# Performance work log

Hardware: AMD Instinct MI355X
Metric: run time of the kernel (lower is better)

## Reference

```python
import jax, jax.numpy as jnp
import numpy as np

B, T, H = 16, 2048, 1024   # batch, time, hidden_dim
G, V, D = 2, 320, 128      # num_codebooks, codebook_size, codebook_dim
TAU = 1.0                  # gumbel-softmax temperature (forward default)
EPS = 1e-9


def setup_inputs() -> dict:
    key = jax.random.key(0)
    ks = jax.random.split(key, 6)
    return {
        "x": jax.random.normal(ks[0], (B, T, H), jnp.float32),
        "W_in": jax.random.normal(ks[1], (G * V, H), jnp.float32) / np.sqrt(H),
        "b_in": jnp.zeros((G * V,), jnp.float32),
        "codebook": jax.random.uniform(ks[2], (G, V, D), jnp.float32),
        "W_out": jax.random.normal(ks[3], (H, G * D), jnp.float32) / np.sqrt(G * D),
        "b_out": jnp.zeros((H,), jnp.float32),
        "gumbel_u": jax.random.uniform(ks[4], (B, T, G, V), jnp.float32,
                                       minval=1e-6, maxval=1.0 - 1e-6),
    }


def reference(x, W_in, b_in, codebook, W_out, b_out, gumbel_u):
    # input projection -> per-group logits [B,T,G,V]
    logits = (x @ W_in.T + b_in).reshape(B, T, G, V)
    # gumbel-softmax (soft, training path)
    gumbels = -jnp.log(-jnp.log(gumbel_u))
    probs = jax.nn.softmax((logits + gumbels) / TAU, axis=-1)
    # perplexity over average code usage
    avg_probs = probs.mean(axis=(0, 1))  # [G,V]
    perplexity = jnp.exp(-(avg_probs * jnp.log(avg_probs + EPS)).sum(-1)).mean()
    # quantize: soft mixture over codebook, concat groups, project out
    q = jnp.einsum('btgv,gvd->btgd', probs, codebook).reshape(B, T, G * D)
    q = q @ W_out.T + b_out  # [B,T,H]
    commit_loss = jnp.mean((x - jax.lax.stop_gradient(q)) ** 2)
    return (q, perplexity, commit_loss)
```

## Files before the change

kernel.cpp:

```cpp
#include <hip/hip_runtime.h>

typedef unsigned short ushort_t;
typedef unsigned int uint_t;
typedef __attribute__((ext_vector_type(4))) float f32x4;
typedef __attribute__((ext_vector_type(8))) short bf16x8;

#define B_   16
#define T_   2048
#define H_   1024
#define G_   2
#define V_   320
#define D_   128
#define NT   32768
#define GV   640
#define GD   256

#define LGKM0() asm volatile("s_waitcnt lgkmcnt(0)" ::: "memory")
#define BAR()   __builtin_amdgcn_s_barrier()
#define GLDS16(g, l) __builtin_amdgcn_global_load_lds( \
    (const __attribute__((address_space(1))) void*)(g), \
    (__attribute__((address_space(3))) void*)(l), 16, 0, 0)

__device__ __forceinline__ ushort_t cvt_bf16(float f) {
  uint_t u = __float_as_uint(f);
  uint_t r = (u + 0x7FFFu + ((u >> 16) & 1u)) >> 16;
  return (ushort_t)r;
}

__device__ __forceinline__ bf16x8 pack8(f32x4 a, f32x4 b) {
  union { uint_t u[4]; bf16x8 v; } r;
  asm("v_cvt_pk_bf16_f32 %0, %1, %2" : "=v"(r.u[0]) : "v"(a[0]), "v"(a[1]));
  asm("v_cvt_pk_bf16_f32 %0, %1, %2" : "=v"(r.u[1]) : "v"(a[2]), "v"(a[3]));
  asm("v_cvt_pk_bf16_f32 %0, %1, %2" : "=v"(r.u[2]) : "v"(b[0]), "v"(b[1]));
  asm("v_cvt_pk_bf16_f32 %0, %1, %2" : "=v"(r.u[3]) : "v"(b[2]), "v"(b[3]));
  return r.v;
}

__global__ void pq_prep(const float* __restrict__ W_in, const float* __restrict__ W_out,
                        const float* __restrict__ cb, ushort_t* __restrict__ winb,
                        ushort_t* __restrict__ woutb, ushort_t* __restrict__ cbp,
                        float* __restrict__ avg_g, float* __restrict__ closs,
                        uint_t* __restrict__ counter) {
  int idx = blockIdx.x * 256 + threadIdx.x;
  const int N1 = GV * H_;
  const int N2 = H_ * GD;
  const int N3 = 81920;
  if (idx < N1) { winb[idx] = cvt_bf16(W_in[idx]); return; }
  idx -= N1;
  if (idx < N2) { woutb[idx] = cvt_bf16(W_out[idx]); return; }
  idx -= N2;
  if (idx < N3) {
    int g = idx / 40960;
    int r = idx % 40960;
    int kk = r / 4096;
    int r2 = r % 4096;
    int n  = r2 >> 9;
    int ln = (r2 >> 3) & 63;
    int i  = r2 & 7;
    int v = kk * 32 + (ln >> 4) * 8 + i;
    int d = n * 16 + (ln & 15);
    cbp[idx] = cvt_bf16(cb[((size_t)g * V_ + v) * D_ + d]);
    return;
  }
  idx -= N3;
  if (idx < GV) { avg_g[idx] = 0.f; return; }
  idx -= GV;
  if (idx == 0) { *closs = 0.f; *counter = 0u; }
}

__global__ __launch_bounds__(512, 2) void pq_kA(
    const float* __restrict__ x, const float* __restrict__ b_in,
    const float* __restrict__ gum, const ushort_t* __restrict__ winb,
    const ushort_t* __restrict__ cbp, ushort_t* __restrict__ qmid,
    float* __restrict__ avg_g) {
  __shared__ char smem[117248];
  char* sAbuf = smem;
  char* sBbuf = smem + 32768;
  char* sP    = smem;
  float* sAvg = (float*)(smem + 114688);

  const int tid = threadIdx.x;
  const int lane = tid & 63;
  const int wid = tid >> 6;
  const int wm = wid >> 1;
  const int g  = wid & 1;
  const int lo = lane & 15;
  const int hi = lane >> 4;
  const int row0 = blockIdx.x * 128;

  for (int i = tid; i < GV; i += 512) sAvg[i] = 0.f;

  const int aR   = (wid << 4) + (lane >> 3);
  const int aCc  = (lane & 7) ^ (lane >> 3);
  const float* aSrc0 = x + (size_t)(row0 + aR) * H_ + aCc * 4;
  const int bV   = wid * 80 + (lane >> 2);
  const int bCc  = (lane & 3) ^ ((lane >> 3) & 3);
  const ushort_t* bSrc0 = winb + (size_t)bV * H_ + bCc * 8;

  f32x4 acc[2][20];
#pragma unroll
  for (int m = 0; m < 2; ++m)
#pragma unroll
    for (int n = 0; n < 20; ++n) acc[m][n] = (f32x4){0.f, 0.f, 0.f, 0.f};

  __syncthreads();

#define STAGE(buf, kb)                                                          \
  do {                                                                          \
    char* la = sAbuf + (buf) * 16384 + wid * 2048;                              \
    char* lb = sBbuf + (buf) * 40960 + wid * 5120;                              \
    const float* as = aSrc0 + (kb);                                             \
    GLDS16(as,            la);                                                  \
    GLDS16(as + 8 * H_,   la + 1024);                                           \
    const ushort_t* bs = bSrc0 + (kb);                                          \
    GLDS16(bs,             lb);                                                 \
    GLDS16(bs + 16 * H_,   lb + 1024);                                          \
    GLDS16(bs + 32 * H_,   lb + 2048);                                          \
    GLDS16(bs + 48 * H_,   lb + 3072);                                          \
    GLDS16(bs + 64 * H_,   lb + 4096);                                          \
  } while (0)

  STAGE(0, 0);

  const int swzA = lo & 7;
  const int swzB = (lo >> 1) & 3;

#pragma unroll 1
  for (int ks = 0; ks < 32; ++ks) {
    const int cur = ks & 1;
    if (ks < 31) {
      STAGE(cur ^ 1, (ks + 1) * 32);
      asm volatile("s_waitcnt vmcnt(7)" ::: "memory");
    } else {
      asm volatile("s_waitcnt vmcnt(0)" ::: "memory");
    }
    BAR();

    const char* cA = sAbuf + cur * 16384;
    const char* cB = sBbuf + cur * 40960;
    bf16x8 af[2];
#pragma unroll
    for (int m = 0; m < 2; ++m) {
      const int row = wm * 32 + m * 16 + lo;
      const int rb = row * 128;
      f32x4 a0 = *reinterpret_cast<const f32x4*>(cA + rb + (((hi * 2)     ^ swzA) * 16));
      f32x4 a1 = *reinterpret_cast<const f32x4*>(cA + rb + (((hi * 2 + 1) ^ swzA) * 16));
      af[m] = pack8(a0, a1);
    }
#pragma unroll
    for (int n = 0; n < 20; ++n) {
      const int v = g * 320 + n * 16 + lo;
      bf16x8 bf = *reinterpret_cast<const bf16x8*>(cB + v * 64 + ((hi ^ swzB) * 16));
      acc[0][n] = __builtin_amdgcn_mfma_f32_16x16x32_bf16(af[0], bf, acc[0][n], 0, 0, 0);
      acc[1][n] = __builtin_amdgcn_mfma_f32_16x16x32_bf16(af[1], bf, acc[1][n], 0, 0, 0);
    }
    LGKM0();
    BAR();
  }
#undef STAGE

  float bias[20];
#pragma unroll
  for (int n = 0; n < 20; ++n) bias[n] = b_in[g * 320 + n * 16 + lo];

#pragma unroll
  for (int mrep = 0; mrep < 2; ++mrep) {
#pragma unroll
    for (int j = 0; j < 4; ++j) {
      const int trow = row0 + wm * 32 + mrep * 16 + hi * 4 + j;
      const float* up = gum + ((size_t)trow * G_ + g) * V_;
      float zmax = -3.0e38f;
#pragma unroll
      for (int n = 0; n < 20; ++n) {
        float u = up[n * 16 + lo];
        float gv = -__logf(-__logf(u));
        float z = acc[mrep][n][j] + bias[n] + gv;
        acc[mrep][n][j] = z;
        zmax = fmaxf(zmax, z);
      }
#pragma unroll
      for (int mk = 1; mk <= 8; mk <<= 1) zmax = fmaxf(zmax, __shfl_xor(zmax, mk));
      float s = 0.f;
#pragma unroll
      for (int n = 0; n < 20; ++n) {
        float p = __expf(acc[mrep][n][j] - zmax);
        acc[mrep][n][j] = p;
        s += p;
      }
#pragma unroll
      for (int mk = 1; mk <= 8; mk <<= 1) s += __shfl_xor(s, mk);
      float inv = 1.f / s;
#pragma unroll
      for (int n = 0; n < 20; ++n) acc[mrep][n][j] *= inv;
    }
#pragma unroll
    for (int n = 0; n < 20; ++n) {
      float cs = acc[mrep][n][0] + acc[mrep][n][1] + acc[mrep][n][2] + acc[mrep][n][3];
      cs += __shfl_xor(cs, 16);
      cs += __shfl_xor(cs, 32);
      if (hi == 0) atomicAdd(&sAvg[g * 320 + n * 16 + lo], cs);
    }
#pragma unroll
    for (int n = 0; n < 20; ++n) {
#pragma unroll
      for (int j = 0; j < 4; ++j) {
        float v = acc[mrep][n][j];
        float pv = __shfl_xor(v, 1);
        if ((lane & 1) == 0) {
          uint_t w = (uint_t)cvt_bf16(v) | ((uint_t)cvt_bf16(pv) << 16);
          int prow = wm * 16 + hi * 4 + j;
          int byte = (prow * 1280 + (g * 320 + n * 16 + lo) * 2) ^ ((prow & 7) << 4);
          *reinterpret_cast<uint_t*>(sP + byte) = w;
        }
      }
    }
    LGKM0();
    f32x4 acc2[8];
#pragma unroll
    for (int n = 0; n < 8; ++n) acc2[n] = (f32x4){0.f, 0.f, 0.f, 0.f};
#pragma unroll
    for (int kk = 0; kk < 10; ++kk) {
      int prow = wm * 16 + lo;
      int byte = (prow * 1280 + g * 640 + kk * 64 + hi * 16) ^ ((prow & 7) << 4);
      bf16x8 ap = *reinterpret_cast<const bf16x8*>(sP + byte);
#pragma unroll
      for (int n = 0; n < 8; ++n) {
        bf16x8 bc = *reinterpret_cast<const bf16x8*>(cbp + ((size_t)((g * 10 + kk) * 8 + n) * 64 + lane) * 8);
        acc2[n] = __builtin_amdgcn_mfma_f32_16x16x32_bf16(ap, bc, acc2[n], 0, 0, 0);
      }
    }
#pragma unroll
    for (int n = 0; n < 8; ++n) {
#pragma unroll
      for (int j = 0; j < 4; ++j) {
        float v = acc2[n][j];
        float pv = __shfl_xor(v, 1);
        if ((lane & 1) == 0) {
          uint_t w = (uint_t)cvt_bf16(v) | ((uint_t)cvt_bf16(pv) << 16);
          int trow = row0 + wm * 32 + mrep * 16 + hi * 4 + j;
          *reinterpret_cast<uint_t*>(qmid + (size_t)trow * GD + g * 128 + n * 16 + lo) = w;
        }
      }
    }
  }
  __syncthreads();
  for (int i = tid; i < GV; i += 512) atomicAdd(&avg_g[i], sAvg[i]);
}

__global__ __launch_bounds__(512, 2) void pq_kB(
    const ushort_t* __restrict__ qmid, const ushort_t* __restrict__ woutb,
    const float* __restrict__ b_out, const float* __restrict__ x,
    float* __restrict__ out, float* __restrict__ closs,
    const float* __restrict__ avg_g, uint_t* __restrict__ counter) {
  __shared__ char smem[49152 + 64];
  __shared__ int sLast;
  char* sA = smem;
  char* sB = smem + 16384;
  float* sRed = (float*)(smem + 49152);

  const int tid = threadIdx.x;
  const int lane = tid & 63;
  const int wid = tid >> 6;
  const int wm = wid >> 2;
  const int wn = wid & 3;
  const int lo = lane & 15, hi = lane >> 4;
  const int tm = blockIdx.x >> 2;
  const int tn = blockIdx.x & 3;
  const int row0 = tm * 128;
  const int col0 = tn * 256;

  f32x4 acc[4][4];
#pragma unroll
  for (int mr = 0; mr < 4; ++mr)
#pragma unroll
    for (int nr = 0; nr < 4; ++nr) acc[mr][nr] = (f32x4){0.f, 0.f, 0.f, 0.f};

  for (int ks = 0; ks < 4; ++ks) {
    const int kb = ks * 64;
#pragma unroll
    for (int u = 0; u < 2; ++u) {
      int s = u * 512 + tid;
      int r = s >> 3, c = s & 7;
      uint4 wv = *reinterpret_cast<const uint4*>(qmid + (size_t)(row0 + r) * GD + kb + c * 8);
      int byte = (r * 128 + c * 16) ^ ((r & 7) << 4);
      *reinterpret_cast<uint4*>(sA + byte) = wv;
    }
#pragma unroll
    for (int u = 0; u < 4; ++u) {
      int s = u * 512 + tid;
      int r = s >> 3, c = s & 7;
      uint4 wv = *reinterpret_cast<const uint4*>(woutb + (size_t)(col0 + r) * GD + kb + c * 8);
      int byte = (r * 128 + c * 16) ^ ((r & 7) << 4);
      *reinterpret_cast<uint4*>(sB + byte) = wv;
    }
    __syncthreads();
#pragma unroll
    for (int kk = 0; kk < 2; ++kk) {
      bf16x8 af[4], bf[4];
#pragma unroll
      for (int mr = 0; mr < 4; ++mr) {
        int row = wm * 64 + mr * 16 + lo;
        int byte = (row * 128 + kk * 64 + hi * 16) ^ ((row & 7) << 4);
        af[mr] = *reinterpret_cast<const bf16x8*>(sA + byte);
      }
#pragma unroll
      for (int nr = 0; nr < 4; ++nr) {
        int col = wn * 64 + nr * 16 + lo;
        int byte = (col * 128 + kk * 64 + hi * 16) ^ ((col & 7) << 4);
        bf[nr] = *reinterpret_cast<const bf16x8*>(sB + byte);
      }
#pragma unroll
      for (int mr = 0; mr < 4; ++mr)
#pragma unroll
        for (int nr = 0; nr < 4; ++nr)
          acc[mr][nr] = __builtin_amdgcn_mfma_f32_16x16x32_bf16(af[mr], bf[nr], acc[mr][nr], 0, 0, 0);
    }
    __syncthreads();
  }
  float bias[4];
#pragma unroll
  for (int nr = 0; nr < 4; ++nr) bias[nr] = b_out[col0 + wn * 64 + nr * 16 + lo];
  float csum = 0.f;
#pragma unroll
  for (int mr = 0; mr < 4; ++mr)
#pragma unroll
    for (int nr = 0; nr < 4; ++nr)
#pragma unroll
      for (int j = 0; j < 4; ++j) {
        int row = row0 + wm * 64 + mr * 16 + hi * 4 + j;
        int col = col0 + wn * 64 + nr * 16 + lo;
        float q = acc[mr][nr][j] + bias[nr];
        out[(size_t)row * H_ + col] = q;
        float d = x[(size_t)row * H_ + col] - q;
        csum += d * d;
      }
#pragma unroll
  for (int mk = 1; mk <= 32; mk <<= 1) csum += __shfl_xor(csum, mk);
  if (lane == 0) sRed[wid] = csum;
  __syncthreads();
  if (tid == 0) {
    float t = 0.f;
    for (int w = 0; w < 8; ++w) t += sRed[w];
    atomicAdd(closs, t);
    __threadfence();
    uint_t c = atomicAdd(counter, 1u);
    sLast = (c == 1023u) ? 1 : 0;
  }
  __syncthreads();
  if (sLast && tid < 64) {
    float a0 = 0.f, a1 = 0.f;
    for (int v = tid; v < V_; v += 64) {
      float p0 = avg_g[v] * (1.f / (float)NT);
      a0 += p0 * __logf(p0 + 1e-9f);
      float p1 = avg_g[V_ + v] * (1.f / (float)NT);
      a1 += p1 * __logf(p1 + 1e-9f);
    }
#pragma unroll
    for (int mk = 1; mk <= 32; mk <<= 1) { a0 += __shfl_xor(a0, mk); a1 += __shfl_xor(a1, mk); }
    if (tid == 0) {
      float cl = atomicAdd(closs, 0.0f);
      out[(size_t)NT * H_]     = 0.5f * (__expf(-a0) + __expf(-a1));
      out[(size_t)NT * H_ + 1] = cl * (1.f / ((float)NT * (float)H_));
    }
  }
}

extern "C" void kernel_launch(void* const* d_in, const int* in_sizes, int n_in,
                              void* d_out, int out_size, void* d_ws, size_t ws_size,
                              hipStream_t stream) {
  const float* x     = (const float*)d_in[0];
  const float* W_in  = (const float*)d_in[1];
  const float* b_in  = (const float*)d_in[2];
  const float* cb    = (const float*)d_in[3];
  const float* W_out = (const float*)d_in[4];
  const float* b_out = (const float*)d_in[5];
  const float* gum   = (const float*)d_in[6];
  float* out = (float*)d_out;

  char* ws = (char*)d_ws;
  ushort_t* winb  = (ushort_t*)ws;
  ushort_t* woutb = (ushort_t*)(ws + 1310720);
  ushort_t* cbp   = (ushort_t*)(ws + 1835008);
  float*    avg_g = (float*)(ws + 1998848);
  float*    closs = (float*)(ws + 2001408);
  uint_t*   cnt   = (uint_t*)(ws + 2001472);
  ushort_t* qmid  = (ushort_t*)(ws + 2001920);

  pq_prep<<<3907, 256, 0, stream>>>(W_in, W_out, cb, winb, woutb, cbp, avg_g, closs, cnt);
  pq_kA<<<256, 512, 0, stream>>>(x, b_in, gum, winb, cbp, qmid, avg_g);
  pq_kB<<<1024, 512, 0, stream>>>(qmid, woutb, b_out, x, out, closs, avg_g, cnt);
}
```

Baseline: 235.5 us.

## Load x tiles directly into registers and triple-buffer the W_in LDS stages

The x operand of the input GEMM now goes from global memory straight into registers, one k-step ahead, instead of through a swizzled LDS staging buffer. The freed LDS space triple-buffers the bf16 W_in tiles, so B loads run two k-steps ahead under adjusted vmcnt waits. This is meant to cut LDS traffic and give the B operand more latency hiding. In exchange, each x prefetch must land within one iteration, the per-lane strided global reads may coalesce less well, and the larger LDS footprint may limit occupancy.

```diff
diff --git a/kernel.cpp b/kernel.cpp
--- a/kernel.cpp
+++ b/kernel.cpp
@@ -73,11 +73,10 @@
     const float* __restrict__ gum, const ushort_t* __restrict__ winb,
     const ushort_t* __restrict__ cbp, ushort_t* __restrict__ qmid,
     float* __restrict__ avg_g) {
-  __shared__ char smem[117248];
-  char* sAbuf = smem;
-  char* sBbuf = smem + 32768;
+  __shared__ char smem[125440];
+  char* sBbuf = smem;
   char* sP    = smem;
-  float* sAvg = (float*)(smem + 114688);
+  float* sAvg = (float*)(smem + 122880);
 
   const int tid = threadIdx.x;
   const int lane = tid & 63;
@@ -90,13 +89,13 @@
 
   for (int i = tid; i < GV; i += 512) sAvg[i] = 0.f;
 
-  const int aR   = (wid << 4) + (lane >> 3);
-  const int aCc  = (lane & 7) ^ (lane >> 3);
-  const float* aSrc0 = x + (size_t)(row0 + aR) * H_ + aCc * 4;
   const int bV   = wid * 80 + (lane >> 2);
   const int bCc  = (lane & 3) ^ ((lane >> 3) & 3);
   const ushort_t* bSrc0 = winb + (size_t)bV * H_ + bCc * 8;
 
+  const float* xr0 = x + (size_t)(row0 + wm * 32 + lo) * H_ + hi * 8;
+  const float* xr1 = xr0 + (size_t)16 * H_;
+
   f32x4 acc[2][20];
 #pragma unroll
   for (int m = 0; m < 2; ++m)
@@ -105,13 +104,9 @@
 
   __syncthreads();
 
-#define STAGE(buf, kb)                                                          \
+#define STAGEB(buf, kb)                                                         \
   do {                                                                          \
-    char* la = sAbuf + (buf) * 16384 + wid * 2048;                              \
     char* lb = sBbuf + (buf) * 40960 + wid * 5120;                              \
-    const float* as = aSrc0 + (kb);                                             \
-    GLDS16(as,            la);                                                  \
-    GLDS16(as + 8 * H_,   la + 1024);                                           \
     const ushort_t* bs = bSrc0 + (kb);                                          \
     GLDS16(bs,             lb);                                                 \
     GLDS16(bs + 16 * H_,   lb + 1024);                                          \
@@ -120,44 +115,45 @@
     GLDS16(bs + 64 * H_,   lb + 4096);                                          \
   } while (0)
 
-  STAGE(0, 0);
-
-  const int swzA = lo & 7;
+  STAGEB(0, 0);
+  f32x4 xa0 = *reinterpret_cast<const f32x4*>(xr0);
+  f32x4 xa1 = *reinterpret_cast<const f32x4*>(xr0 + 4);
+  f32x4 xb0 = *reinterpret_cast<const f32x4*>(xr1);
+  f32x4 xb1 = *reinterpret_cast<const f32x4*>(xr1 + 4);
+  STAGEB(1, 32);
+
   const int swzB = (lo >> 1) & 3;
 
 #pragma unroll 1
   for (int ks = 0; ks < 32; ++ks) {
-    const int cur = ks & 1;
+    if (ks < 31) asm volatile("s_waitcnt vmcnt(5)" ::: "memory");
+    else         asm volatile("s_waitcnt vmcnt(0)" ::: "memory");
+    BAR();
+
+    bf16x8 af0 = pack8(xa0, xa1);
+    bf16x8 af1 = pack8(xb0, xb1);
+
     if (ks < 31) {
-      STAGE(cur ^ 1, (ks + 1) * 32);
-      asm volatile("s_waitcnt vmcnt(7)" ::: "memory");
-    } else {
-      asm volatile("s_waitcnt vmcnt(0)" ::: "memory");
-    }
-    BAR();
-
-    const char* cA = sAbuf + cur * 16384;
-    const char* cB = sBbuf + cur * 40960;
-    bf16x8 af[2];
-#pragma unroll
-    for (int m = 0; m < 2; ++m) {
-      const int row = wm * 32 + m * 16 + lo;
-      const int rb = row * 128;
-      f32x4 a0 = *reinterpret_cast<const f32x4*>(cA + rb + (((hi * 2)     ^ swzA) * 16));
-      f32x4 a1 = *reinterpret_cast<const f32x4*>(cA + rb + (((hi * 2 + 1) ^ swzA) * 16));
-      af[m] = pack8(a0, a1);
-    }
+      const int ko = (ks + 1) * 32;
+      xa0 = *reinterpret_cast<const f32x4*>(xr0 + ko);
+      xa1 = *reinterpret_cast<const f32x4*>(xr0 + ko + 4);
+      xb0 = *reinterpret_cast<const f32x4*>(xr1 + ko);
+      xb1 = *reinterpret_cast<const f32x4*>(xr1 + ko + 4);
+      if (ks < 30) STAGEB((ks + 2) % 3, (ks + 2) * 32);
+    }
+
+    const char* cB = sBbuf + (ks % 3) * 40960;
 #pragma unroll
     for (int n = 0; n < 20; ++n) {
       const int v = g * 320 + n * 16 + lo;
       bf16x8 bf = *reinterpret_cast<const bf16x8*>(cB + v * 64 + ((hi ^ swzB) * 16));
-      acc[0][n] = __builtin_amdgcn_mfma_f32_16x16x32_bf16(af[0], bf, acc[0][n], 0, 0, 0);
-      acc[1][n] = __builtin_amdgcn_mfma_f32_16x16x32_bf16(af[1], bf, acc[1][n], 0, 0, 0);
+      acc[0][n] = __builtin_amdgcn_mfma_f32_16x16x32_bf16(af0, bf, acc[0][n], 0, 0, 0);
+      acc[1][n] = __builtin_amdgcn_mfma_f32_16x16x32_bf16(af1, bf, acc[1][n], 0, 0, 0);
     }
     LGKM0();
     BAR();
   }
-#undef STAGE
+#undef STAGEB
 
   float bias[20];
 #pragma unroll
```

After: 255.1 us. 1.08x slower.
